# Performance work log

Hardware: AMD Instinct MI355X
Metric: run time of the kernel (lower is better)

Reference implementation:

```python
import jax, jax.numpy as jnp
import numpy as np


def setup_inputs() -> dict:
    key = jax.random.key(0)
    k1, k2, k3, k4 = jax.random.split(key, 4)
    S, B, C, H, W = 5, 16, 11, 128, 128  # S = nstack + 1
    NCLASS, F = 11, 7
    return {
        "heat_preds": jax.random.normal(k1, (S, B, C, H, W), dtype=jnp.float32),
        "heatmaps": jax.random.normal(k2, (S, B, C, H, W), dtype=jnp.float32),
        "label_preds": jax.random.normal(k3, (S, B, NCLASS, F), dtype=jnp.float32),
        "labels": jax.random.normal(k4, (B, NCLASS, F), dtype=jnp.float32),
    }


def reference(heat_preds, heatmaps, label_preds, labels):
    # HeatmapLoss per stack: mean over H,W then sum over C -> [S, B]
    heat_l = jnp.mean((heat_preds - heatmaps) ** 2, axis=(3, 4)).sum(axis=2)
    combined_loss = heat_l.T  # [B, S] == torch.stack(list, dim=1)

    # LabelLoss per stack: sum of squared error over first 7 feats and classes -> [S, B]
    diff = label_preds[:, :, :, :7] - labels[None, :, :, :7]  # [S, B, nclass, 7]
    labels_loss = (diff ** 2).sum(axis=(2, 3)).T  # [B, S]

    return (combined_loss, labels_loss)
```

## Files before the change

### kernel.cpp

```cpp
#include <hip/hip_runtime.h>

#define SS 5
#define BB 16
#define CC 11
#define HW 16384
#define CF 77

__global__ void init_and_labels_kernel(const float* __restrict__ label_preds,
                                       const float* __restrict__ labels,
                                       float* __restrict__ out) {
    int t = threadIdx.x;
    if (t < SS * BB) {
        int s = t / BB;
        int b = t % BB;
        out[b * SS + s] = 0.0f;
        const float* lp = label_preds + (size_t)(s * BB + b) * CF;
        const float* lb = labels + (size_t)b * CF;
        float sum = 0.0f;
#pragma unroll
        for (int i = 0; i < CF; ++i) {
            float d = lp[i] - lb[i];
            sum += d * d;
        }
        out[SS * BB + b * SS + s] = sum;
    }
}

__global__ __launch_bounds__(256) void heat_loss_kernel(const float* __restrict__ hp,
                                                        const float* __restrict__ hm,
                                                        float* __restrict__ out) {
    const int blk = blockIdx.x;
    const int b = (blk / CC) % BB;
    const int s = blk / (BB * CC);
    const size_t base = (size_t)blk * HW;

    const float4* __restrict__ p = (const float4*)(hp + base);
    const float4* __restrict__ q = (const float4*)(hm + base);

    const int t = threadIdx.x;
    float sum = 0.0f;
#pragma unroll
    for (int i = 0; i < HW / 4 / 256; ++i) {
        float4 a = p[t + i * 256];
        float4 m = q[t + i * 256];
        float d0 = a.x - m.x;
        float d1 = a.y - m.y;
        float d2 = a.z - m.z;
        float d3 = a.w - m.w;
        sum += d0 * d0 + d1 * d1 + d2 * d2 + d3 * d3;
    }

#pragma unroll
    for (int off = 32; off > 0; off >>= 1) sum += __shfl_down(sum, off, 64);

    __shared__ float ws[4];
    const int lane = t & 63;
    const int wave = t >> 6;
    if (lane == 0) ws[wave] = sum;
    __syncthreads();
    if (t == 0) {
        float tot = ws[0] + ws[1] + ws[2] + ws[3];
        atomicAdd(&out[b * SS + s], tot * (1.0f / (float)HW));
    }
}

extern "C" void kernel_launch(void* const* d_in, const int* in_sizes, int n_in,
                              void* d_out, int out_size, void* d_ws, size_t ws_size,
                              hipStream_t stream) {
    const float* heat_preds = (const float*)d_in[0];
    const float* heatmaps = (const float*)d_in[1];
    const float* label_preds = (const float*)d_in[2];
    const float* labels = (const float*)d_in[3];
    float* out = (float*)d_out;

    init_and_labels_kernel<<<1, 128, 0, stream>>>(label_preds, labels, out);

    heat_loss_kernel<<<SS * BB * CC, 256, 0, stream>>>(heat_preds, heatmaps, out);
}
```

Measured before the change: 138.6 us.

## Split heatmap reduction into chunked partials with a deterministic final reduce kernel

Measured after the change: 131.9 us. -4.8%, faster.

```diff
diff --git a/kernel.cpp b/kernel.cpp
--- a/kernel.cpp
+++ b/kernel.cpp
@@ -5,42 +5,23 @@
 #define CC 11
 #define HW 16384
 #define CF 77
+#define CHUNK 4096
+#define NCHUNK 4
+#define NPART (SS * BB * CC * NCHUNK)
+#define PPO (CC * NCHUNK)
 
-__global__ void init_and_labels_kernel(const float* __restrict__ label_preds,
-                                       const float* __restrict__ labels,
-                                       float* __restrict__ out) {
-    int t = threadIdx.x;
-    if (t < SS * BB) {
-        int s = t / BB;
-        int b = t % BB;
-        out[b * SS + s] = 0.0f;
-        const float* lp = label_preds + (size_t)(s * BB + b) * CF;
-        const float* lb = labels + (size_t)b * CF;
-        float sum = 0.0f;
-#pragma unroll
-        for (int i = 0; i < CF; ++i) {
-            float d = lp[i] - lb[i];
-            sum += d * d;
-        }
-        out[SS * BB + b * SS + s] = sum;
-    }
-}
-
-__global__ __launch_bounds__(256) void heat_loss_kernel(const float* __restrict__ hp,
-                                                        const float* __restrict__ hm,
-                                                        float* __restrict__ out) {
+__global__ __launch_bounds__(256) void heat_partial_kernel(const float* __restrict__ hp,
+                                                           const float* __restrict__ hm,
+                                                           float* __restrict__ partials) {
     const int blk = blockIdx.x;
-    const int b = (blk / CC) % BB;
-    const int s = blk / (BB * CC);
-    const size_t base = (size_t)blk * HW;
-
+    const size_t base = (size_t)blk * CHUNK;
     const float4* __restrict__ p = (const float4*)(hp + base);
     const float4* __restrict__ q = (const float4*)(hm + base);
 
     const int t = threadIdx.x;
     float sum = 0.0f;
 #pragma unroll
-    for (int i = 0; i < HW / 4 / 256; ++i) {
+    for (int i = 0; i < CHUNK / 4 / 256; ++i) {
         float4 a = p[t + i * 256];
         float4 m = q[t + i * 256];
         float d0 = a.x - m.x;
@@ -53,14 +34,47 @@
 #pragma unroll
     for (int off = 32; off > 0; off >>= 1) sum += __shfl_down(sum, off, 64);
 
-    __shared__ float ws[4];
+    __shared__ float wsum[4];
     const int lane = t & 63;
     const int wave = t >> 6;
-    if (lane == 0) ws[wave] = sum;
+    if (lane == 0) wsum[wave] = sum;
     __syncthreads();
-    if (t == 0) {
-        float tot = ws[0] + ws[1] + ws[2] + ws[3];
-        atomicAdd(&out[b * SS + s], tot * (1.0f / (float)HW));
+    if (t == 0) partials[blk] = wsum[0] + wsum[1] + wsum[2] + wsum[3];
+}
+
+__global__ __launch_bounds__(64) void final_kernel(const float* __restrict__ partials,
+                                                   const float* __restrict__ label_preds,
+                                                   const float* __restrict__ labels,
+                                                   float* __restrict__ out) {
+    const int sb = blockIdx.x;
+    const int s = sb / BB;
+    const int b = sb % BB;
+    const int lane = threadIdx.x;
+
+    float h = (lane < PPO) ? partials[sb * PPO + lane] : 0.0f;
+
+    const float* lp = label_preds + (size_t)sb * CF;
+    const float* lb = labels + (size_t)b * CF;
+    float l = 0.0f;
+    if (lane < CF) {
+        float d = lp[lane] - lb[lane];
+        l = d * d;
+    }
+    const int i2 = lane + 64;
+    if (i2 < CF) {
+        float d = lp[i2] - lb[i2];
+        l += d * d;
+    }
+
+#pragma unroll
+    for (int off = 32; off > 0; off >>= 1) {
+        h += __shfl_down(h, off, 64);
+        l += __shfl_down(l, off, 64);
+    }
+
+    if (lane == 0) {
+        out[b * SS + s] = h * (1.0f / (float)HW);
+        out[SS * BB + b * SS + s] = l;
     }
 }
 
@@ -72,8 +86,8 @@
     const float* label_preds = (const float*)d_in[2];
     const float* labels = (const float*)d_in[3];
     float* out = (float*)d_out;
+    float* partials = (float*)d_ws;
 
-    init_and_labels_kernel<<<1, 128, 0, stream>>>(label_preds, labels, out);
-
-    heat_loss_kernel<<<SS * BB * CC, 256, 0, stream>>>(heat_preds, heatmaps, out);
+    heat_partial_kernel<<<NPART, 256, 0, stream>>>(heat_preds, heatmaps, partials);
+    final_kernel<<<SS * BB, 64, 0, stream>>>(partials, label_preds, labels, out);
 }
```
